# Kernel optimization log

Hardware: AMD Instinct MI355X
Metric: run time of the kernel (lower is better)

Reference implementation:

```python
import jax, jax.numpy as jnp
import numpy as np

BATCH = 4096
IN_DIMS = (128, 128)   # input spatial dims (H, W)
W_DIMS = (16, 16)      # weight_dims from init_kwargs


def setup_inputs() -> dict:
    key = jax.random.key(0)
    k1, k2 = jax.random.split(key)
    inputs = jax.random.normal(k1, (BATCH,) + IN_DIMS, dtype=jnp.float32)
    w = jax.random.normal(k2, W_DIMS, dtype=jnp.float32)
    return {"inputs": inputs, "w": w}


def reference(inputs, w):
    # GTPCA_Layer.call_input_larger with project=True (shift transform,
    # input dims strictly larger than weight dims).
    B, H, W = inputs.shape
    kh, kw = w.shape
    n = jnp.asarray(H * W, dtype=inputs.dtype)  # self.n = prod(input_dims)

    # weights = w / sqrt(sum(w^2) / n)
    wn = w / jnp.sqrt(jnp.sum(w * w) / n)

    # scores = valid cross-correlation(inputs, wn) / n  -> (B, H-kh+1, W-kw+1)
    scores = jax.lax.conv_general_dilated(
        inputs[:, None, :, :], wn[None, None, :, :],
        window_strides=(1, 1), padding='VALID',
        dimension_numbers=('NCHW', 'OIHW', 'NCHW'))[:, 0] / n
    sh, sw = scores.shape[1], scores.shape[2]

    # first-occurrence argmax of |scores| over spatial dims (matches the
    # cumsum <= 1 trick in get_argmax: jnp.argmax returns first max)
    flat_abs = jnp.abs(scores).reshape(B, -1)
    idx = jnp.argmax(flat_abs, axis=-1)          # (B,)
    rows = idx // sw
    cols = idx % sw

    # gather_nd(scores, argmax, batch_dims=1)
    smax = jnp.take_along_axis(scores.reshape(B, -1), idx[:, None], axis=-1)[:, 0]

    # per-sample dynamic pad of wn to input_dims with offset = argmax
    # (tf.map_fn(tf.pad(weights, [argmax, max_argmax-argmax-1])))
    def pad_one(r, c):
        return jax.lax.dynamic_update_slice(
            jnp.zeros((H, W), dtype=inputs.dtype), wn, (r, c))

    wpad = jax.vmap(pad_one)(rows, cols)         # (B, H, W)

    # output = score_at_argmax * padded weights
    return smax[:, None, None] * wpad
```

## Files before the change

### kernel.cpp

```cpp
#include <hip/hip_runtime.h>
#include <math.h>

#define H 128
#define SW 113
#define CAND_CAP 96

typedef __attribute__((ext_vector_type(8))) short short8;
typedef __attribute__((ext_vector_type(4))) float f32x4;

static __device__ __forceinline__ uint32_t f2bf1(float v) {
    uint32_t u = __float_as_uint(v);
    return (u + 0x7fffu + ((u >> 16) & 1u)) >> 16;
}
static __device__ __forceinline__ uint32_t pack2(float a, float b) {
    return f2bf1(a) | (f2bf1(b) << 16);
}
static __device__ __forceinline__ float bf2f(unsigned short v) {
    return __uint_as_float(((uint32_t)v) << 16);
}

__global__ __launch_bounds__(256) void prep_wn(const float* __restrict__ w,
                                               float* __restrict__ wn) {
    __shared__ float red[256];
    int t = threadIdx.x;
    float wv = w[t];
    red[t] = wv * wv;
    __syncthreads();
    for (int off = 128; off > 0; off >>= 1) {
        if (t < off) red[t] += red[t + off];
        __syncthreads();
    }
    float denom = sqrtf(red[0] / 16384.0f);
    wn[t] = wv / denom;
}

__global__ __launch_bounds__(256) void gtpca_main(
    const float* __restrict__ in, const float* __restrict__ wn_g,
    float* __restrict__ out) {

    __shared__ __align__(16) uint32_t lds[15424];
    uint32_t* lds_in = lds;
    uint32_t* lds_sc = lds + 8192;
    float* red_a  = (float*)lds;
    int*   cand_n = (int*)(lds + 256);
    int*   cand_i = (int*)(lds + 260);
    float* cand_v = (float*)(lds + 260 + CAND_CAP);

    const int tid  = threadIdx.x;
    const int lane = tid & 63;
    const int wid  = tid >> 6;
    const int b    = blockIdx.x;
    const float* ip  = in + (size_t)b * (H * H);
    const float4* in4 = (const float4*)ip;

    const int n15 = lane & 15;
    const int kg  = lane >> 4;
    short8 Breg[16];
#pragma unroll
    for (int ki = 0; ki < 16; ++ki) {
        short8 f;
#pragma unroll
        for (int e = 0; e < 8; ++e) {
            int d = kg * 8 + e - n15;
            float v = ((unsigned)d < 16u) ? wn_g[ki * 16 + d] : 0.0f;
            f[e] = (short)f2bf1(v);
        }
        Breg[ki] = f;
    }

#pragma unroll
    for (int i = 0; i < 16; ++i) {
        int g = tid + 256 * i;
        float4 v = in4[g];
        int r = g >> 5, h = g & 31;
        int phys = (h >> 1) ^ (r & 7);
        uint2 pk = make_uint2(pack2(v.x, v.y), pack2(v.z, v.w));
        *(uint2*)(lds_in + r * 64 + phys * 4 + (h & 1) * 2) = pk;
    }
    __syncthreads();

    const short8* ldsA = (const short8*)lds_in;
#pragma unroll
    for (int tyi = 0; tyi < 2; ++tyi) {
        int ty = 2 * wid + tyi;
        int rbase = 16 * ty + n15;
#pragma unroll
        for (int hf = 0; hf < 2; ++hf) {
            f32x4 C[4];
            f32x4 Cz = {0.0f, 0.0f, 0.0f, 0.0f};
#pragma unroll
            for (int j = 0; j < 4; ++j) C[j] = Cz;
#pragma unroll
            for (int ki = 0; ki < 16; ++ki) {
                int r = rbase + ki; if (r > 127) r = 127;
                int rx = r << 4, rk = r & 7;
#pragma unroll
                for (int j = 0; j < 4; ++j) {
                    int cl = 2 * (4 * hf + j) + kg;
                    if (cl > 15) cl = 15;
                    short8 a = ldsA[rx | (cl ^ rk)];
                    C[j] = __builtin_amdgcn_mfma_f32_16x16x32_bf16(a, Breg[ki], C[j], 0, 0, 0);
                }
            }
            int ys  = 16 * ty + 4 * kg;
            int cch = ys >> 3;
#pragma unroll
            for (int j = 0; j < 4; ++j) {
                int x = 16 * (4 * hf + j) + n15;
                if (x < SW) {
                    uint2 pk = make_uint2(pack2(C[j][0], C[j][1]),
                                          pack2(C[j][2], C[j][3]));
                    *(uint2*)(lds_sc + x * 64 + ((cch ^ (x & 15)) << 2) + (kg & 1) * 2) = pk;
                }
            }
        }
    }
    __syncthreads();

    const int sx = tid >> 1;
    const int c0 = (tid & 1) * 8;
    float best_a = -1.0f;
    if (sx < SW) {
#pragma unroll
        for (int q = 0; q < 8; ++q) {
            int cch = c0 + q;
            short8 v = *(const short8*)(lds_sc + sx * 64 + ((cch ^ (sx & 15)) << 2));
#pragma unroll
            for (int e = 0; e < 8; ++e) {
                int y = cch * 8 + e;
                float a = fabsf(bf2f((unsigned short)v[e]));
                if (y < SW && a > best_a) best_a = a;
            }
        }
    }
    if (tid == 0) *cand_n = 0;
    red_a[tid] = best_a;
    __syncthreads();
    for (int off = 128; off > 0; off >>= 1) {
        if (tid < off) red_a[tid] = fmaxf(red_a[tid], red_a[tid + off]);
        __syncthreads();
    }
    const float tau = red_a[0] - 48.0f;

    if (sx < SW) {
#pragma unroll
        for (int q = 0; q < 8; ++q) {
            int cch = c0 + q;
            short8 v = *(const short8*)(lds_sc + sx * 64 + ((cch ^ (sx & 15)) << 2));
#pragma unroll
            for (int e = 0; e < 8; ++e) {
                int y = cch * 8 + e;
                float a = fabsf(bf2f((unsigned short)v[e]));
                if (y < SW && a >= tau) {
                    int pos = atomicAdd(cand_n, 1);
                    if (pos < CAND_CAP) cand_i[pos] = y * SW + sx;
                }
            }
        }
    }
    __syncthreads();
    int ncand = *cand_n; if (ncand > CAND_CAP) ncand = CAND_CAP;

    for (int c = wid; c < ncand; c += 4) {
        int idx = cand_i[c];
        int yy = idx / SW, xx = idx - yy * SW;
        int kj = lane & 15, k0 = (lane >> 4) * 4;
        float s = 0.0f;
#pragma unroll
        for (int j2 = 0; j2 < 4; ++j2) {
            int ki = k0 + j2;
            s = __builtin_fmaf(ip[(yy + ki) * H + xx + kj], wn_g[ki * 16 + kj], s);
        }
#pragma unroll
        for (int mk = 32; mk > 0; mk >>= 1) s += __shfl_xor(s, mk, 64);
        if (lane == 0) cand_v[c] = s;
    }
    __syncthreads();

    float bsa = -1.0f, bsv = 0.0f; int bsi = 0x7FFFFFFF;
    for (int c = 0; c < ncand; ++c) {
        float v = cand_v[c], a = fabsf(v);
        int idx = cand_i[c];
        if (a > bsa || (a == bsa && idx < bsi)) { bsa = a; bsi = idx; bsv = v; }
    }
    const int rr = bsi / SW;
    const int cc = bsi - rr * SW;
    const float sv = bsv * (1.0f / 16384.0f);

    float4* out4 = (float4*)(out + (size_t)b * (H * H));
#pragma unroll
    for (int i = 0; i < 16; ++i) {
        int g = tid + i * 256;
        int orow = g >> 5;
        int ocol = (g & 31) << 2;
        float4 v = {0.0f, 0.0f, 0.0f, 0.0f};
        int dr = orow - rr;
        if ((unsigned)dr < 16u) {
            float* vp = (float*)&v;
#pragma unroll
            for (int k = 0; k < 4; ++k) {
                int dc = ocol + k - cc;
                if ((unsigned)dc < 16u) vp[k] = sv * wn_g[dr * 16 + dc];
            }
        }
        out4[g] = v;
    }
}

extern "C" void kernel_launch(void* const* d_in, const int* in_sizes, int n_in,
                              void* d_out, int out_size, void* d_ws, size_t ws_size,
                              hipStream_t stream) {
    const float* in = (const float*)d_in[0];
    const float* w = (const float*)d_in[1];
    float* out = (float*)d_out;
    float* wn = (float*)d_ws;

    prep_wn<<<1, 256, 0, stream>>>(w, wn);
    gtpca_main<<<4096, 256, 0, stream>>>(in, wn, out);
}
```

Before: 515.1 us.

## Keep conv scores in registers instead of LDS to cut LDS footprint

The bf16 score tile no longer goes to LDS. Each thread computes its running max of |score| directly from the MFMA accumulators and keeps the packed bf16 scores in a 32-entry register array for the candidate-selection pass. This shrinks LDS from about 60KB to 32KB, and a launch-bounds hint asks for 3 blocks per CU, aiming at higher occupancy and fewer LDS round trips. In exchange it raises register pressure, and the candidate cap grows to 128. The max now uses fp32 values while the candidate test uses bf16-rounded values, which could slightly change which entries qualify.

```diff
diff --git a/kernel.cpp b/kernel.cpp
--- a/kernel.cpp
+++ b/kernel.cpp
@@ -3,7 +3,7 @@
 
 #define H 128
 #define SW 113
-#define CAND_CAP 96
+#define CAND_CAP 128
 
 typedef __attribute__((ext_vector_type(8))) short short8;
 typedef __attribute__((ext_vector_type(4))) float f32x4;
@@ -15,8 +15,11 @@
 static __device__ __forceinline__ uint32_t pack2(float a, float b) {
     return f2bf1(a) | (f2bf1(b) << 16);
 }
-static __device__ __forceinline__ float bf2f(unsigned short v) {
-    return __uint_as_float(((uint32_t)v) << 16);
+static __device__ __forceinline__ float bf2f_lo(uint32_t d) {
+    return __uint_as_float(d << 16);
+}
+static __device__ __forceinline__ float bf2f_hi(uint32_t d) {
+    return __uint_as_float(d & 0xffff0000u);
 }
 
 __global__ __launch_bounds__(256) void prep_wn(const float* __restrict__ w,
@@ -34,13 +37,11 @@
     wn[t] = wv / denom;
 }
 
-__global__ __launch_bounds__(256) void gtpca_main(
+__global__ __launch_bounds__(256, 3) void gtpca_main(
     const float* __restrict__ in, const float* __restrict__ wn_g,
     float* __restrict__ out) {
 
-    __shared__ __align__(16) uint32_t lds[15424];
-    uint32_t* lds_in = lds;
-    uint32_t* lds_sc = lds + 8192;
+    __shared__ __align__(16) uint32_t lds[8192];
     float* red_a  = (float*)lds;
     int*   cand_n = (int*)(lds + 256);
     int*   cand_i = (int*)(lds + 260);
@@ -74,12 +75,14 @@
         float4 v = in4[g];
         int r = g >> 5, h = g & 31;
         int phys = (h >> 1) ^ (r & 7);
-        uint2 pk = make_uint2(pack2(v.x, v.y), pack2(v.z, v.w));
-        *(uint2*)(lds_in + r * 64 + phys * 4 + (h & 1) * 2) = pk;
-    }
-    __syncthreads();
-
-    const short8* ldsA = (const short8*)lds_in;
+        uint2 pk2 = make_uint2(pack2(v.x, v.y), pack2(v.z, v.w));
+        *(uint2*)(lds + r * 64 + phys * 4 + (h & 1) * 2) = pk2;
+    }
+    __syncthreads();
+
+    const short8* ldsA = (const short8*)lds;
+    uint32_t pk[32];
+    float best_a = -1.0f;
 #pragma unroll
     for (int tyi = 0; tyi < 2; ++tyi) {
         int ty = 2 * wid + tyi;
@@ -102,39 +105,29 @@
                     C[j] = __builtin_amdgcn_mfma_f32_16x16x32_bf16(a, Breg[ki], C[j], 0, 0, 0);
                 }
             }
-            int ys  = 16 * ty + 4 * kg;
-            int cch = ys >> 3;
+            int ybase = 16 * ty + 4 * kg;
 #pragma unroll
             for (int j = 0; j < 4; ++j) {
                 int x = 16 * (4 * hf + j) + n15;
                 if (x < SW) {
-                    uint2 pk = make_uint2(pack2(C[j][0], C[j][1]),
-                                          pack2(C[j][2], C[j][3]));
-                    *(uint2*)(lds_sc + x * 64 + ((cch ^ (x & 15)) << 2) + (kg & 1) * 2) = pk;
+#pragma unroll
+                    for (int ri = 0; ri < 4; ++ri) {
+                        int y = ybase + ri;
+                        if (y < SW) {
+                            float a = fabsf(C[j][ri]);
+                            if (a > best_a) best_a = a;
+                        }
+                    }
                 }
-            }
-        }
-    }
-    __syncthreads();
-
-    const int sx = tid >> 1;
-    const int c0 = (tid & 1) * 8;
-    float best_a = -1.0f;
-    if (sx < SW) {
-#pragma unroll
-        for (int q = 0; q < 8; ++q) {
-            int cch = c0 + q;
-            short8 v = *(const short8*)(lds_sc + sx * 64 + ((cch ^ (sx & 15)) << 2));
-#pragma unroll
-            for (int e = 0; e < 8; ++e) {
-                int y = cch * 8 + e;
-                float a = fabsf(bf2f((unsigned short)v[e]));
-                if (y < SW && a > best_a) best_a = a;
-            }
-        }
-    }
+                pk[((tyi * 2 + hf) * 4 + j) * 2 + 0] = pack2(C[j][0], C[j][1]);
+                pk[((tyi * 2 + hf) * 4 + j) * 2 + 1] = pack2(C[j][2], C[j][3]);
+            }
+        }
+    }
+    __syncthreads();
+
+    red_a[tid] = best_a;
     if (tid == 0) *cand_n = 0;
-    red_a[tid] = best_a;
     __syncthreads();
     for (int off = 128; off > 0; off >>= 1) {
         if (tid < off) red_a[tid] = fmaxf(red_a[tid], red_a[tid + off]);
@@ -142,18 +135,30 @@
     }
     const float tau = red_a[0] - 48.0f;
 
-    if (sx < SW) {
-#pragma unroll
-        for (int q = 0; q < 8; ++q) {
-            int cch = c0 + q;
-            short8 v = *(const short8*)(lds_sc + sx * 64 + ((cch ^ (sx & 15)) << 2));
-#pragma unroll
-            for (int e = 0; e < 8; ++e) {
-                int y = cch * 8 + e;
-                float a = fabsf(bf2f((unsigned short)v[e]));
-                if (y < SW && a >= tau) {
-                    int pos = atomicAdd(cand_n, 1);
-                    if (pos < CAND_CAP) cand_i[pos] = y * SW + sx;
+#pragma unroll
+    for (int tyi = 0; tyi < 2; ++tyi) {
+#pragma unroll
+        for (int hf = 0; hf < 2; ++hf) {
+#pragma unroll
+            for (int j = 0; j < 4; ++j) {
+                int x = 16 * (4 * hf + j) + n15;
+                if (x < SW) {
+                    int ybase = 16 * (2 * wid + tyi) + 4 * kg;
+#pragma unroll
+                    for (int p = 0; p < 2; ++p) {
+                        uint32_t d = pk[((tyi * 2 + hf) * 4 + j) * 2 + p];
+                        float v0 = bf2f_lo(d);
+                        float v1 = bf2f_hi(d);
+                        int y0 = ybase + 2 * p;
+                        if (y0 < SW && fabsf(v0) >= tau) {
+                            int pos = atomicAdd(cand_n, 1);
+                            if (pos < CAND_CAP) cand_i[pos] = y0 * SW + x;
+                        }
+                        if (y0 + 1 < SW && fabsf(v1) >= tau) {
+                            int pos = atomicAdd(cand_n, 1);
+                            if (pos < CAND_CAP) cand_i[pos] = (y0 + 1) * SW + x;
+                        }
+                    }
                 }
             }
         }
```

Measured after the change: 580.2 us. 1.13x slower.
